# Kernel optimization log

Measured on AMD Instinct MI355X. Metric: run time of the kernel, lower is better.

## Reference

```python
import jax, jax.numpy as jnp
import numpy as np

NUM_NEIGHBORS = 10
BN_EPS = 1e-5


def setup_inputs() -> dict:
    key = jax.random.key(0)
    ks = jax.random.split(key, 6)
    B, N, D = 8, 4096, 64
    x = jax.random.normal(ks[0], (B, N, D), jnp.float32)

    def w(k, shape):
        return jax.random.normal(k, shape, jnp.float32) * 0.05

    return {
        "x": x,
        "gamma": jnp.ones((D,), jnp.float32),
        "beta": jnp.zeros((D,), jnp.float32),
        "W1": w(ks[1], (128, 128)), "b1": jnp.zeros((128,), jnp.float32),
        "W2": w(ks[2], (128, 64)), "b2": jnp.zeros((64,), jnp.float32),
        "W3": w(ks[3], (64, 64)), "b3": jnp.zeros((64,), jnp.float32),
        "Wg": w(ks[4], (128, 64)), "bg": jnp.zeros((64,), jnp.float32),
    }


def reference(x, gamma, beta, W1, b1, W2, b2, W3, b3, Wg, bg):
    B, N, D = x.shape
    K = NUM_NEIGHBORS

    # BatchNorm1d in train mode: normalize over all B*N rows with batch stats
    xf = x.reshape(-1, D)
    mu = jnp.mean(xf, axis=0)
    var = jnp.mean((xf - mu) ** 2, axis=0)  # biased, as torch BN uses
    xn = (((xf - mu) / jnp.sqrt(var + BN_EPS)) * gamma + beta).reshape(B, N, D)

    # KNN in feature space (standard DGCNN gather_neighbours)
    sq = jnp.sum(xn * xn, axis=-1)  # [B,N]
    dist = sq[:, :, None] + sq[:, None, :] - 2.0 * jnp.einsum("bnd,bmd->bnm", xn, xn)
    _, idx = jax.lax.top_k(-dist, K)  # [B,N,K] indices of nearest (incl. self)

    # gather neighbor features: neigh[b,n,k,:] = xn[b, idx[b,n,k], :]
    neigh = jax.vmap(lambda f, i: f[i])(xn, idx)  # [B,N,K,D]

    exp = jnp.broadcast_to(xn[:, :, None, :], (B, N, K, D))
    edge = jnp.concatenate([exp, exp - neigh], axis=-1)  # [B,N,K,2D]

    h = jax.nn.relu(edge @ W1 + b1)
    h = jax.nn.relu(h @ W2 + b2)
    h = jax.nn.relu(h @ W3 + b3)  # [B,N,K,64]

    vert = jnp.max(h, axis=2)  # max over neighbors -> [B,N,64]
    g = jnp.max(vert, axis=1, keepdims=True)  # global max-pool [B,1,64]
    cat = jnp.concatenate([vert, jnp.broadcast_to(g, vert.shape)], axis=-1)  # [B,N,128]
    return jax.nn.relu(cat @ Wg + bg)  # [B,N,64]
```

## Files before the change

### kernel.cpp

```cpp
#include <hip/hip_runtime.h>
#include <hip/hip_fp16.h>
#include <float.h>

#define BB 8
#define NN 4096
#define DD 64
#define KNBR 10
#define ROWS (BB*NN)

typedef _Float16 f16x8 __attribute__((ext_vector_type(8)));
typedef float f32x4 __attribute__((ext_vector_type(4)));

__global__ void k_bn_stats(const float* __restrict__ x, float* __restrict__ stats) {
  __shared__ float ls[2][4][64];
  int d = threadIdx.x & 63;
  int g = threadIdx.x >> 6;
  float s = 0.f, s2 = 0.f;
  for (int r = blockIdx.x * 4 + g; r < ROWS; r += gridDim.x * 4) {
    float val = x[r * 64 + d];
    s += val;
    s2 = fmaf(val, val, s2);
  }
  ls[0][g][d] = s;
  ls[1][g][d] = s2;
  __syncthreads();
  if (g == 0) {
    atomicAdd(&stats[d],      ls[0][0][d] + ls[0][1][d] + ls[0][2][d] + ls[0][3][d]);
    atomicAdd(&stats[64 + d], ls[1][0][d] + ls[1][1][d] + ls[1][2][d] + ls[1][3][d]);
  }
}

__global__ void k_bn_finalize(const float* __restrict__ stats,
                              const float* __restrict__ gamma,
                              const float* __restrict__ beta,
                              float* __restrict__ ss) {
  int d = threadIdx.x;
  const float inv = 1.f / 32768.f;
  float mu  = stats[d] * inv;
  float var = stats[64 + d] * inv - mu * mu;
  float sc  = gamma[d] / sqrtf(var + 1e-5f);
  ss[d]      = sc;
  ss[64 + d] = beta[d] - mu * sc;
}

__global__ void k_normalize(const float* __restrict__ x, const float* __restrict__ ss,
                            float* __restrict__ xn, float* __restrict__ sq,
                            _Float16* __restrict__ xh, _Float16* __restrict__ xl) {
  int row = blockIdx.x * 4 + (threadIdx.x >> 6);
  int d = threadIdx.x & 63;
  int idx = row * 64 + d;
  float val = fmaf(x[idx], ss[d], ss[64 + d]);
  xn[idx] = val;
  _Float16 h = (_Float16)val;
  _Float16 l = (_Float16)(val - (float)h);
  xh[idx] = h;
  xl[idx] = l;
  float p = val * val;
  #pragma unroll
  for (int off = 32; off > 0; off >>= 1) p += __shfl_xor(p, off);
  if (d == 0) sq[row] = p;
}

__global__ __launch_bounds__(256, 2) void k_knn(const _Float16* __restrict__ xh,
                                                const _Float16* __restrict__ xl,
                                                const float* __restrict__ sq,
                                                int* __restrict__ knn) {
  __shared__ __align__(16) float lds[16640];
  const int tid = threadIdx.x;
  const int w = tid >> 6, lane = tid & 63;
  const int l15 = lane & 15, lg = lane >> 4;
  const int b = blockIdx.x >> 6;
  const int rowbase = (blockIdx.x & 63) << 6;
  const int bN = b * NN;
  const _Float16* __restrict__ xhb = xh + (size_t)bN * 64;
  const _Float16* __restrict__ xlb = xl + (size_t)bN * 64;

  char* wbase = (char*)lds + w * 16640;
  char* Bhi = wbase;
  char* Blo = wbase + 4096;
  float* Dw = (float*)(wbase + 8192);

  f16x8 Ah[4][2], Al[4][2];
  #pragma unroll
  for (int mt = 0; mt < 4; ++mt) {
    #pragma unroll
    for (int ks = 0; ks < 2; ++ks) {
      int r = rowbase + mt * 16 + l15;
      Ah[mt][ks] = *(const f16x8*)(xhb + r * 64 + ks * 32 + lg * 8);
      Al[mt][ks] = *(const f16x8*)(xlb + r * 64 + ks * 32 + lg * 8);
    }
  }

  float bd[10]; int bi[10];
  #pragma unroll
  for (int i = 0; i < 10; ++i) { bd[i] = FLT_MAX; bi[i] = 0; }

  int srow[4], scc[4];
  #pragma unroll
  for (int i = 0; i < 4; ++i) { int c = i * 64 + lane; srow[i] = c >> 3; scc[i] = c & 7; }

  f16x8 sh[4], sl[4];
  {
    int mb0 = w * 32;
    #pragma unroll
    for (int i = 0; i < 4; ++i) {
      sh[i] = *(const f16x8*)(xhb + (mb0 + srow[i]) * 64 + scc[i] * 8);
      sl[i] = *(const f16x8*)(xlb + (mb0 + srow[i]) * 64 + scc[i] * 8);
    }
  }

  float* Drow = Dw + lane * 33;

  #pragma unroll 1
  for (int t = 0; t < 32; ++t) {
    const int mb = (t * 4 + w) * 32;
    const int mb2 = (t < 31) ? ((t + 1) * 4 + w) * 32 : mb;
    float sqv0 = sq[bN + mb + l15];
    float sqv1 = sq[bN + mb + 16 + l15];
    #pragma unroll
    for (int i = 0; i < 4; ++i) {
      int off = srow[i] * 128 + 16 * (scc[i] ^ (srow[i] & 7));
      *(f16x8*)(Bhi + off) = sh[i];
      *(f16x8*)(Blo + off) = sl[i];
    }
    #pragma unroll
    for (int i = 0; i < 4; ++i) {
      sh[i] = *(const f16x8*)(xhb + (mb2 + srow[i]) * 64 + scc[i] * 8);
      sl[i] = *(const f16x8*)(xlb + (mb2 + srow[i]) * 64 + scc[i] * 8);
    }
    f16x8 Bh[2][2], Bl[2][2];
    #pragma unroll
    for (int nt = 0; nt < 2; ++nt) {
      #pragma unroll
      for (int ks = 0; ks < 2; ++ks) {
        int rr2 = nt * 16 + l15;
        int off = rr2 * 128 + 16 * ((ks * 4 + lg) ^ (rr2 & 7));
        Bh[nt][ks] = *(const f16x8*)(Bhi + off);
        Bl[nt][ks] = *(const f16x8*)(Blo + off);
      }
    }
    #pragma unroll
    for (int mt = 0; mt < 4; ++mt) {
      f32x4 a0 = {0.f, 0.f, 0.f, 0.f}, a1 = {0.f, 0.f, 0.f, 0.f};
      #pragma unroll
      for (int ks = 0; ks < 2; ++ks) {
        a0 = __builtin_amdgcn_mfma_f32_16x16x32_f16(Ah[mt][ks], Bh[0][ks], a0, 0, 0, 0);
        a1 = __builtin_amdgcn_mfma_f32_16x16x32_f16(Ah[mt][ks], Bh[1][ks], a1, 0, 0, 0);
        a0 = __builtin_amdgcn_mfma_f32_16x16x32_f16(Ah[mt][ks], Bl[0][ks], a0, 0, 0, 0);
        a1 = __builtin_amdgcn_mfma_f32_16x16x32_f16(Ah[mt][ks], Bl[1][ks], a1, 0, 0, 0);
        a0 = __builtin_amdgcn_mfma_f32_16x16x32_f16(Al[mt][ks], Bh[0][ks], a0, 0, 0, 0);
        a1 = __builtin_amdgcn_mfma_f32_16x16x32_f16(Al[mt][ks], Bh[1][ks], a1, 0, 0, 0);
      }
      int rw = mt * 16 + lg * 4;
      #pragma unroll
      for (int r2 = 0; r2 < 4; ++r2) {
        Dw[(rw + r2) * 33 + l15]      = fmaf(-2.f, a0[r2], sqv0);
        Dw[(rw + r2) * 33 + 16 + l15] = fmaf(-2.f, a1[r2], sqv1);
      }
    }
    #pragma unroll 4
    for (int mm = 0; mm < 32; ++mm) {
      float dv = Drow[mm];
      if (dv < bd[9]) {
        float cd = dv; int ci = bN + mb + mm;
        #pragma unroll
        for (int j = 0; j < 10; ++j) {
          bool swp = cd < bd[j];
          float tf = bd[j]; int ti = bi[j];
          bd[j] = swp ? cd : tf; bi[j] = swp ? ci : ti;
          cd = swp ? tf : cd;    ci = swp ? ti : ci;
        }
      }
    }
  }

  __syncthreads();
  float* md = lds;
  int*   mi = (int*)(lds + 2560);
  #pragma unroll
  for (int i = 0; i < 10; ++i) {
    md[(w * 64 + lane) * 10 + i] = bd[i];
    mi[(w * 64 + lane) * 10 + i] = bi[i];
  }
  __syncthreads();
  if (tid < 64) {
    float fd[10]; int fi[10];
    #pragma unroll
    for (int i = 0; i < 10; ++i) { fd[i] = FLT_MAX; fi[i] = 0; }
    for (int w2 = 0; w2 < 4; ++w2) {
      for (int kk = 0; kk < 10; ++kk) {
        float dd2 = md[(w2 * 64 + tid) * 10 + kk];
        int   ii2 = mi[(w2 * 64 + tid) * 10 + kk];
        if (dd2 < fd[9]) {
          float cd = dd2; int ci = ii2;
          #pragma unroll
          for (int j = 0; j < 10; ++j) {
            bool swp = cd < fd[j];
            float tf = fd[j]; int ti = fi[j];
            fd[j] = swp ? cd : tf; fi[j] = swp ? ci : ti;
            cd = swp ? tf : cd;    ci = swp ? ti : ci;
          }
        }
      }
    }
    #pragma unroll
    for (int kk = 0; kk < 10; ++kk)
      knn[(bN + rowbase + tid) * KNBR + kk] = fi[kk];
  }
}

__global__ void k_uv(const float* __restrict__ xn, const float* __restrict__ W1,
                     const float* __restrict__ b1, float* __restrict__ u,
                     float* __restrict__ v) {
  __shared__ float xs[64 * 64];
  const int tid = threadIdx.x;
  const int o = tid & 127;
  const bool isU = tid < 128;
  const int rowbase = blockIdx.x * 64;

  float wreg[64];
  #pragma unroll
  for (int d = 0; d < 64; ++d) {
    float bw = W1[(64 + d) * 128 + o];
    wreg[d] = isU ? (W1[d * 128 + o] + bw) : bw;
  }
  const float bb = isU ? b1[o] : 0.f;
  float* __restrict__ dst = isU ? u : v;

  {
    const float4* s4 = (const float4*)(xn + rowbase * 64);
    float4* d4 = (float4*)xs;
    #pragma unroll
    for (int i = 0; i < 4; ++i) d4[tid + 256 * i] = s4[tid + 256 * i];
  }
  __syncthreads();

  for (int r = 0; r < 64; ++r) {
    const float4* xr = (const float4*)(xs + r * 64);
    float a0 = bb, a1 = 0.f, a2 = 0.f, a3 = 0.f;
    #pragma unroll
    for (int q = 0; q < 16; ++q) {
      float4 xv = xr[q];
      a0 = fmaf(xv.x, wreg[4 * q + 0], a0);
      a1 = fmaf(xv.y, wreg[4 * q + 1], a1);
      a2 = fmaf(xv.z, wreg[4 * q + 2], a2);
      a3 = fmaf(xv.w, wreg[4 * q + 3], a3);
    }
    dst[(rowbase + r) * 128 + o] = (a0 + a1) + (a2 + a3);
  }
}

__global__ __launch_bounds__(256, 2) void k_edge(const float* __restrict__ uu,
                                                 const float* __restrict__ vv,
                                                 const int* __restrict__ knn,
                                                 const float* __restrict__ W2,
                                                 const float* __restrict__ b2,
                                                 const float* __restrict__ W3,
                                                 const float* __restrict__ b3,
                                                 float* __restrict__ vert) {
  __shared__ __align__(16) _Float16 W3Ts[64 * 72];
  __shared__ __align__(16) _Float16 h2buf[4][16 * 88];
  __shared__ int vmaxs[4][512];
  const int tid = threadIdx.x;
  const int w = tid >> 6, lane = tid & 63;
  const int l15 = lane & 15, lg = lane >> 4;

  for (int i = tid; i < 64 * 64; i += 256) {
    int o3 = i >> 6, k2 = i & 63;
    W3Ts[o3 * 72 + k2] = (_Float16)W3[k2 * 64 + o3];
  }
  f16x8 w2f[4][4];
  #pragma unroll
  for (int ks = 0; ks < 4; ++ks) {
    #pragma unroll
    for (int nt = 0; nt < 4; ++nt) {
      f16x8 t;
      #pragma unroll
      for (int j = 0; j < 8; ++j)
        t[j] = (_Float16)W2[(ks * 32 + lg * 8 + j) * 64 + nt * 16 + l15];
      w2f[ks][nt] = t;
    }
  }
  float bias2[4], bias3[4];
  #pragma unroll
  for (int nt = 0; nt < 4; ++nt) { bias2[nt] = b2[nt * 16 + l15]; bias3[nt] = b3[nt * 16 + l15]; }

  _Float16* h2w = h2buf[w];
  int* vmaxw = vmaxs[w];
  #pragma unroll
  for (int q = 0; q < 8; ++q) vmaxw[lane * 8 + q] = 0;
  __syncthreads();

  const int wgid = blockIdx.x * 4 + w;
  for (int j = 0; j < 4; ++j) {
    const int g = wgid * 4 + j;
    const int n0 = g * 8;
    const int ebase = n0 * KNBR;
    #pragma unroll 1
    for (int mt = 0; mt < 5; ++mt) {
      const int e = mt * 16 + l15;
      const int m = knn[ebase + e];
      const int n = n0 + e / 10;
      const float* Up = uu + (size_t)n * 128 + lg * 8;
      const float* Vp = vv + (size_t)m * 128 + lg * 8;
      f16x8 A[4];
      #pragma unroll
      for (int ks = 0; ks < 4; ++ks) {
        float4 ua = *(const float4*)(Up + ks * 32);
        float4 ub = *(const float4*)(Up + ks * 32 + 4);
        float4 va = *(const float4*)(Vp + ks * 32);
        float4 vb = *(const float4*)(Vp + ks * 32 + 4);
        f16x8 t;
        t[0] = (_Float16)fmaxf(ua.x - va.x, 0.f);
        t[1] = (_Float16)fmaxf(ua.y - va.y, 0.f);
        t[2] = (_Float16)fmaxf(ua.z - va.z, 0.f);
        t[3] = (_Float16)fmaxf(ua.w - va.w, 0.f);
        t[4] = (_Float16)fmaxf(ub.x - vb.x, 0.f);
        t[5] = (_Float16)fmaxf(ub.y - vb.y, 0.f);
        t[6] = (_Float16)fmaxf(ub.z - vb.z, 0.f);
        t[7] = (_Float16)fmaxf(ub.w - vb.w, 0.f);
        A[ks] = t;
      }
      f32x4 acc[4];
      #pragma unroll
      for (int nt = 0; nt < 4; ++nt) { float bbv = bias2[nt]; acc[nt] = (f32x4){bbv, bbv, bbv, bbv}; }
      #pragma unroll
      for (int ks = 0; ks < 4; ++ks) {
        #pragma unroll
        for (int nt = 0; nt < 4; ++nt)
          acc[nt] = __builtin_amdgcn_mfma_f32_16x16x32_f16(A[ks], w2f[ks][nt], acc[nt], 0, 0, 0);
      }
      #pragma unroll
      for (int nt = 0; nt < 4; ++nt) {
        #pragma unroll
        for (int r = 0; r < 4; ++r)
          h2w[(lg * 4 + r) * 88 + nt * 16 + l15] = (_Float16)fmaxf(acc[nt][r], 0.f);
      }
      f16x8 A3[2];
      #pragma unroll
      for (int ks2 = 0; ks2 < 2; ++ks2)
        A3[ks2] = *(const f16x8*)(h2w + l15 * 88 + ks2 * 32 + lg * 8);
      f32x4 c3[4];
      #pragma unroll
      for (int nt = 0; nt < 4; ++nt) { float bbv = bias3[nt]; c3[nt] = (f32x4){bbv, bbv, bbv, bbv}; }
      #pragma unroll
      for (int ks2 = 0; ks2 < 2; ++ks2) {
        #pragma unroll
        for (int nt = 0; nt < 4; ++nt) {
          f16x8 bf = *(const f16x8*)(W3Ts + (nt * 16 + l15) * 72 + ks2 * 32 + lg * 8);
          c3[nt] = __builtin_amdgcn_mfma_f32_16x16x32_f16(A3[ks2], bf, c3[nt], 0, 0, 0);
        }
      }
      #pragma unroll
      for (int nt = 0; nt < 4; ++nt) {
        #pragma unroll
        for (int r = 0; r < 4; ++r) {
          float val = fmaxf(c3[nt][r], 0.f);
          int e2 = mt * 16 + lg * 4 + r;
          int p = e2 / 10;
          atomicMax(&vmaxw[p * 64 + nt * 16 + l15], __float_as_int(val));
        }
      }
    }
    {
      int p2 = lane >> 3, c0 = (lane & 7) * 8;
      const int* vp = &vmaxw[p2 * 64 + c0];
      float4 r0, r1;
      r0.x = __int_as_float(vp[0]); r0.y = __int_as_float(vp[1]);
      r0.z = __int_as_float(vp[2]); r0.w = __int_as_float(vp[3]);
      r1.x = __int_as_float(vp[4]); r1.y = __int_as_float(vp[5]);
      r1.z = __int_as_float(vp[6]); r1.w = __int_as_float(vp[7]);
      *(float4*)(vert + (size_t)(n0 + p2) * 64 + c0) = r0;
      *(float4*)(vert + (size_t)(n0 + p2) * 64 + c0 + 4) = r1;
      #pragma unroll
      for (int q = 0; q < 8; ++q) vmaxw[lane * 8 + q] = 0;
    }
  }
}

__global__ void k_gmax(const float* __restrict__ vert, float* __restrict__ g) {
  __shared__ float red[4][64];
  int b = blockIdx.x >> 4, chunk = blockIdx.x & 15;
  int sub = threadIdx.x >> 6, o = threadIdx.x & 63;
  float vm = 0.f;
  for (int j = 0; j < 64; ++j) {
    int r = chunk * 256 + j * 4 + sub;
    vm = fmaxf(vm, vert[(b * NN + r) * 64 + o]);
  }
  red[sub][o] = vm;
  __syncthreads();
  if (sub == 0) {
    float mm = fmaxf(fmaxf(red[0][o], red[1][o]), fmaxf(red[2][o], red[3][o]));
    atomicMax((int*)&g[b * 64 + o], __float_as_int(mm));
  }
}

__global__ void k_gb(const float* __restrict__ g, const float* __restrict__ Wg,
                     const float* __restrict__ bg, float* __restrict__ gb) {
  int t = threadIdx.x;
  int b = t >> 6, o = t & 63;
  float acc = bg[o];
  #pragma unroll
  for (int i = 0; i < 64; ++i)
    acc = fmaf(g[b * 64 + i], Wg[(64 + i) * 64 + o], acc);
  gb[b * 64 + o] = acc;
}

__global__ void k_final(const float* __restrict__ vert, const float* __restrict__ Wg,
                        const float* __restrict__ gb, float* __restrict__ out) {
  __shared__ float Wgs[64 * 64];
  int tid = threadIdx.x, w = tid >> 6, lane = tid & 63;
  for (int i = tid; i < 4096; i += 256) Wgs[i] = Wg[i];
  __syncthreads();
  int gw = blockIdx.x * 4 + w;
  for (int j = 0; j < 4; ++j) {
    int n = gw + 8192 * j;
    int b = n >> 12;
    float vrow = vert[n * 64 + lane];
    float ac0 = gb[b * 64 + lane], ac1 = 0.f, ac2 = 0.f, ac3 = 0.f;
    #pragma unroll
    for (int i = 0; i < 64; i += 4) {
      ac0 = fmaf(__shfl(vrow, i),     Wgs[i * 64 + lane],       ac0);
      ac1 = fmaf(__shfl(vrow, i + 1), Wgs[(i + 1) * 64 + lane], ac1);
      ac2 = fmaf(__shfl(vrow, i + 2), Wgs[(i + 2) * 64 + lane], ac2);
      ac3 = fmaf(__shfl(vrow, i + 3), Wgs[(i + 3) * 64 + lane], ac3);
    }
    out[n * 64 + lane] = fmaxf((ac0 + ac1) + (ac2 + ac3), 0.f);
  }
}

extern "C" void kernel_launch(void* const* d_in, const int* in_sizes, int n_in,
                              void* d_out, int out_size, void* d_ws, size_t ws_size,
                              hipStream_t stream) {
  const float* x     = (const float*)d_in[0];
  const float* gamma = (const float*)d_in[1];
  const float* beta  = (const float*)d_in[2];
  const float* W1    = (const float*)d_in[3];
  const float* b1    = (const float*)d_in[4];
  const float* W2    = (const float*)d_in[5];
  const float* b2    = (const float*)d_in[6];
  const float* W3    = (const float*)d_in[7];
  const float* b3    = (const float*)d_in[8];
  const float* Wg    = (const float*)d_in[9];
  const float* bg    = (const float*)d_in[10];
  float* out = (float*)d_out;

  float* ws    = (float*)d_ws;
  float* stats = ws;
  float* ss    = ws + 128;
  float* xn    = ws + 256;
  float* sq    = xn + 2097152;
  int*   knn   = (int*)(sq + 32768);
  float* u     = (float*)(knn + 327680);
  float* v     = u + 4194304;
  float* vert  = v + 4194304;
  float* g     = vert + 2097152;
  float* gb    = g + 512;
  _Float16* xh = (_Float16*)(gb + 512);
  _Float16* xl = (_Float16*)(gb + 512 + 1048576);

  hipMemsetAsync(stats, 0, 128 * sizeof(float), stream);
  hipMemsetAsync(g, 0, 512 * sizeof(float), stream);

  k_bn_stats<<<256, 256, 0, stream>>>(x, stats);
  k_bn_finalize<<<1, 64, 0, stream>>>(stats, gamma, beta, ss);
  k_normalize<<<8192, 256, 0, stream>>>(x, ss, xn, sq, xh, xl);
  k_knn<<<512, 256, 0, stream>>>(xh, xl, sq, knn);
  k_uv<<<512, 256, 0, stream>>>(xn, W1, b1, u, v);
  k_edge<<<256, 256, 0, stream>>>(u, v, knn, W2, b2, W3, b3, vert);
  k_gmax<<<128, 256, 0, stream>>>(vert, g);
  k_gb<<<1, 512, 0, stream>>>(g, Wg, bg, gb);
  k_final<<<2048, 256, 0, stream>>>(vert, Wg, gb, out);
}
```

Measured before the change: 474.9 us.

## Track only top-k distances, then recompute pass to emit neighbor indices

The per-lane top-10 insertion now keeps only distance values, using a branchless min/max network instead of paired value/index swaps, and the cross-wave merge drops index arrays. The 10th-smallest distance becomes a per-row threshold. A second full pass recomputes the MFMA distance tiles and writes every candidate at or below the threshold into the knn output through shared-memory atomic slot counters. This cuts register pressure and the cost of the selection loop, but doubles the distance GEMM work. Neighbor order becomes nondeterministic, and ties at the threshold may drop indices.

Result: no change. 469.3 us (-1.2%).

```diff
diff --git a/kernel.cpp b/kernel.cpp
--- a/kernel.cpp
+++ b/kernel.cpp
@@ -66,6 +66,8 @@
                                                 const float* __restrict__ sq,
                                                 int* __restrict__ knn) {
   __shared__ __align__(16) float lds[16640];
+  __shared__ float thrs[64];
+  __shared__ int cnts[64];
   const int tid = threadIdx.x;
   const int w = tid >> 6, lane = tid & 63;
   const int l15 = lane & 15, lg = lane >> 4;
@@ -91,9 +93,9 @@
     }
   }
 
-  float bd[10]; int bi[10];
-  #pragma unroll
-  for (int i = 0; i < 10; ++i) { bd[i] = FLT_MAX; bi[i] = 0; }
+  float bd[10];
+  #pragma unroll
+  for (int i = 0; i < 10; ++i) bd[i] = FLT_MAX;
 
   int srow[4], scc[4];
   #pragma unroll
@@ -160,15 +162,15 @@
     }
     #pragma unroll 4
     for (int mm = 0; mm < 32; ++mm) {
-      float dv = Drow[mm];
-      if (dv < bd[9]) {
-        float cd = dv; int ci = bN + mb + mm;
+      float cd = Drow[mm];
+      if (cd < bd[9]) {
+        float prev = bd[0];
+        bd[0] = fminf(cd, bd[0]);
         #pragma unroll
-        for (int j = 0; j < 10; ++j) {
-          bool swp = cd < bd[j];
-          float tf = bd[j]; int ti = bi[j];
-          bd[j] = swp ? cd : tf; bi[j] = swp ? ci : ti;
-          cd = swp ? tf : cd;    ci = swp ? ti : ci;
+        for (int j = 1; j < 10; ++j) {
+          float cur = bd[j];
+          bd[j] = fminf(cur, fmaxf(prev, cd));
+          prev = cur;
         }
       }
     }
@@ -176,36 +178,106 @@
 
   __syncthreads();
   float* md = lds;
-  int*   mi = (int*)(lds + 2560);
-  #pragma unroll
-  for (int i = 0; i < 10; ++i) {
-    md[(w * 64 + lane) * 10 + i] = bd[i];
-    mi[(w * 64 + lane) * 10 + i] = bi[i];
-  }
+  #pragma unroll
+  for (int i = 0; i < 10; ++i) md[(w * 64 + lane) * 10 + i] = bd[i];
+  if (tid < 64) cnts[tid] = 0;
   __syncthreads();
   if (tid < 64) {
-    float fd[10]; int fi[10];
-    #pragma unroll
-    for (int i = 0; i < 10; ++i) { fd[i] = FLT_MAX; fi[i] = 0; }
+    float fd[10];
+    #pragma unroll
+    for (int i = 0; i < 10; ++i) fd[i] = FLT_MAX;
     for (int w2 = 0; w2 < 4; ++w2) {
+      #pragma unroll
       for (int kk = 0; kk < 10; ++kk) {
-        float dd2 = md[(w2 * 64 + tid) * 10 + kk];
-        int   ii2 = mi[(w2 * 64 + tid) * 10 + kk];
-        if (dd2 < fd[9]) {
-          float cd = dd2; int ci = ii2;
+        float cd = md[(w2 * 64 + tid) * 10 + kk];
+        if (cd < fd[9]) {
+          float prev = fd[0];
+          fd[0] = fminf(cd, fd[0]);
           #pragma unroll
-          for (int j = 0; j < 10; ++j) {
-            bool swp = cd < fd[j];
-            float tf = fd[j]; int ti = fi[j];
-            fd[j] = swp ? cd : tf; fi[j] = swp ? ci : ti;
-            cd = swp ? tf : cd;    ci = swp ? ti : ci;
+          for (int j = 1; j < 10; ++j) {
+            float cur = fd[j];
+            fd[j] = fminf(cur, fmaxf(prev, cd));
+            prev = cur;
           }
         }
       }
     }
-    #pragma unroll
-    for (int kk = 0; kk < 10; ++kk)
-      knn[(bN + rowbase + tid) * KNBR + kk] = fi[kk];
+    thrs[tid] = fd[9];
+  }
+  __syncthreads();
+
+  float thv[4][4];
+  #pragma unroll
+  for (int mt = 0; mt < 4; ++mt)
+    #pragma unroll
+    for (int r2 = 0; r2 < 4; ++r2)
+      thv[mt][r2] = thrs[mt * 16 + lg * 4 + r2];
+
+  int* knnrow = knn + (size_t)(bN + rowbase) * KNBR;
+
+  {
+    int mb0 = w * 32;
+    #pragma unroll
+    for (int i = 0; i < 4; ++i) {
+      sh[i] = *(const f16x8*)(xhb + (mb0 + srow[i]) * 64 + scc[i] * 8);
+      sl[i] = *(const f16x8*)(xlb + (mb0 + srow[i]) * 64 + scc[i] * 8);
+    }
+  }
+  #pragma unroll 1
+  for (int t = 0; t < 32; ++t) {
+    const int mb = (t * 4 + w) * 32;
+    const int mb2 = (t < 31) ? ((t + 1) * 4 + w) * 32 : mb;
+    float sqv0 = sq[bN + mb + l15];
+    float sqv1 = sq[bN + mb + 16 + l15];
+    #pragma unroll
+    for (int i = 0; i < 4; ++i) {
+      int off = srow[i] * 128 + 16 * (scc[i] ^ (srow[i] & 7));
+      *(f16x8*)(Bhi + off) = sh[i];
+      *(f16x8*)(Blo + off) = sl[i];
+    }
+    #pragma unroll
+    for (int i = 0; i < 4; ++i) {
+      sh[i] = *(const f16x8*)(xhb + (mb2 + srow[i]) * 64 + scc[i] * 8);
+      sl[i] = *(const f16x8*)(xlb + (mb2 + srow[i]) * 64 + scc[i] * 8);
+    }
+    f16x8 Bh[2][2], Bl[2][2];
+    #pragma unroll
+    for (int nt = 0; nt < 2; ++nt) {
+      #pragma unroll
+      for (int ks = 0; ks < 2; ++ks) {
+        int rr2 = nt * 16 + l15;
+        int off = rr2 * 128 + 16 * ((ks * 4 + lg) ^ (rr2 & 7));
+        Bh[nt][ks] = *(const f16x8*)(Bhi + off);
+        Bl[nt][ks] = *(const f16x8*)(Blo + off);
+      }
+    }
+    #pragma unroll
+    for (int mt = 0; mt < 4; ++mt) {
+      f32x4 a0 = {0.f, 0.f, 0.f, 0.f}, a1 = {0.f, 0.f, 0.f, 0.f};
+      #pragma unroll
+      for (int ks = 0; ks < 2; ++ks) {
+        a0 = __builtin_amdgcn_mfma_f32_16x16x32_f16(Ah[mt][ks], Bh[0][ks], a0, 0, 0, 0);
+        a1 = __builtin_amdgcn_mfma_f32_16x16x32_f16(Ah[mt][ks], Bh[1][ks], a1, 0, 0, 0);
+        a0 = __builtin_amdgcn_mfma_f32_16x16x32_f16(Ah[mt][ks], Bl[0][ks], a0, 0, 0, 0);
+        a1 = __builtin_amdgcn_mfma_f32_16x16x32_f16(Ah[mt][ks], Bl[1][ks], a1, 0, 0, 0);
+        a0 = __builtin_amdgcn_mfma_f32_16x16x32_f16(Al[mt][ks], Bh[0][ks], a0, 0, 0, 0);
+        a1 = __builtin_amdgcn_mfma_f32_16x16x32_f16(Al[mt][ks], Bh[1][ks], a1, 0, 0, 0);
+      }
+      #pragma unroll
+      for (int r2 = 0; r2 < 4; ++r2) {
+        float d0 = fmaf(-2.f, a0[r2], sqv0);
+        float d1 = fmaf(-2.f, a1[r2], sqv1);
+        int row = mt * 16 + lg * 4 + r2;
+        if (d0 <= thv[mt][r2]) {
+          int slot = atomicAdd(&cnts[row], 1);
+          if (slot < KNBR) knnrow[row * KNBR + slot] = bN + mb + l15;
+        }
+        if (d1 <= thv[mt][r2]) {
+          int slot = atomicAdd(&cnts[row], 1);
+          if (slot < KNBR) knnrow[row * KNBR + slot] = bN + mb + 16 + l15;
+        }
+      }
+    }
   }
 }
 
```

## Restructure KNN into two-pass threshold search with register-resident distance tiles

Applied to the files above, without the earlier changes.

The KNN kernel now computes distances with candidate rows as the MFMA A operand, so each lane holds 4 distances for one query column directly in registers, with no LDS staging of B tiles or the distance matrix. A first pass keeps only distance values in a fminf/fmaxf insertion network to find each query's 10th-smallest distance threshold. A second pass recomputes the distances and writes the indices at or below the threshold through LDS atomic counters. This drops per-element index bookkeeping and LDS traffic and raises occupancy to 3 blocks per CU, at the cost of doubling the MFMA work. It also drops the ordering of neighbours and the tie handling, which is safe only because the later max over neighbours does not depend on order.

After: 499.2 us. 1.05x slower.

```diff
diff --git a/kernel.cpp b/kernel.cpp
--- a/kernel.cpp
+++ b/kernel.cpp
@@ -61,11 +61,13 @@
   if (d == 0) sq[row] = p;
 }
 
-__global__ __launch_bounds__(256, 2) void k_knn(const _Float16* __restrict__ xh,
+__global__ __launch_bounds__(256, 3) void k_knn(const _Float16* __restrict__ xh,
                                                 const _Float16* __restrict__ xl,
                                                 const float* __restrict__ sq,
                                                 int* __restrict__ knn) {
-  __shared__ __align__(16) float lds[16640];
+  __shared__ float md[64 * 16 * 10];
+  __shared__ float thrs[64];
+  __shared__ int cnts[64];
   const int tid = threadIdx.x;
   const int w = tid >> 6, lane = tid & 63;
   const int l15 = lane & 15, lg = lane >> 4;
@@ -74,138 +76,147 @@
   const int bN = b * NN;
   const _Float16* __restrict__ xhb = xh + (size_t)bN * 64;
   const _Float16* __restrict__ xlb = xl + (size_t)bN * 64;
-
-  char* wbase = (char*)lds + w * 16640;
-  char* Bhi = wbase;
-  char* Blo = wbase + 4096;
-  float* Dw = (float*)(wbase + 8192);
-
-  f16x8 Ah[4][2], Al[4][2];
-  #pragma unroll
-  for (int mt = 0; mt < 4; ++mt) {
+  const float* __restrict__ sqb = sq + bN;
+
+  f16x8 Qh[4][2], Ql[4][2];
+  #pragma unroll
+  for (int nt = 0; nt < 4; ++nt) {
     #pragma unroll
     for (int ks = 0; ks < 2; ++ks) {
-      int r = rowbase + mt * 16 + l15;
-      Ah[mt][ks] = *(const f16x8*)(xhb + r * 64 + ks * 32 + lg * 8);
-      Al[mt][ks] = *(const f16x8*)(xlb + r * 64 + ks * 32 + lg * 8);
-    }
-  }
-
-  float bd[10]; int bi[10];
-  #pragma unroll
-  for (int i = 0; i < 10; ++i) { bd[i] = FLT_MAX; bi[i] = 0; }
-
-  int srow[4], scc[4];
-  #pragma unroll
-  for (int i = 0; i < 4; ++i) { int c = i * 64 + lane; srow[i] = c >> 3; scc[i] = c & 7; }
-
-  f16x8 sh[4], sl[4];
-  {
-    int mb0 = w * 32;
-    #pragma unroll
-    for (int i = 0; i < 4; ++i) {
-      sh[i] = *(const f16x8*)(xhb + (mb0 + srow[i]) * 64 + scc[i] * 8);
-      sl[i] = *(const f16x8*)(xlb + (mb0 + srow[i]) * 64 + scc[i] * 8);
-    }
-  }
-
-  float* Drow = Dw + lane * 33;
+      int qrow = rowbase + nt * 16 + l15;
+      Qh[nt][ks] = *(const f16x8*)(xhb + qrow * 64 + ks * 32 + lg * 8);
+      Ql[nt][ks] = *(const f16x8*)(xlb + qrow * 64 + ks * 32 + lg * 8);
+    }
+  }
+
+  float bd[4][10];
+  #pragma unroll
+  for (int nt = 0; nt < 4; ++nt)
+    #pragma unroll
+    for (int i = 0; i < 10; ++i) bd[nt][i] = FLT_MAX;
+
+  const int mbase0 = w * 1024;
 
   #pragma unroll 1
   for (int t = 0; t < 32; ++t) {
-    const int mb = (t * 4 + w) * 32;
-    const int mb2 = (t < 31) ? ((t + 1) * 4 + w) * 32 : mb;
-    float sqv0 = sq[bN + mb + l15];
-    float sqv1 = sq[bN + mb + 16 + l15];
-    #pragma unroll
-    for (int i = 0; i < 4; ++i) {
-      int off = srow[i] * 128 + 16 * (scc[i] ^ (srow[i] & 7));
-      *(f16x8*)(Bhi + off) = sh[i];
-      *(f16x8*)(Blo + off) = sl[i];
-    }
-    #pragma unroll
-    for (int i = 0; i < 4; ++i) {
-      sh[i] = *(const f16x8*)(xhb + (mb2 + srow[i]) * 64 + scc[i] * 8);
-      sl[i] = *(const f16x8*)(xlb + (mb2 + srow[i]) * 64 + scc[i] * 8);
-    }
-    f16x8 Bh[2][2], Bl[2][2];
-    #pragma unroll
-    for (int nt = 0; nt < 2; ++nt) {
+    const int mb = mbase0 + t * 32;
+    f16x8 Mh[2][2], Ml[2][2];
+    #pragma unroll
+    for (int mt = 0; mt < 2; ++mt) {
       #pragma unroll
       for (int ks = 0; ks < 2; ++ks) {
-        int rr2 = nt * 16 + l15;
-        int off = rr2 * 128 + 16 * ((ks * 4 + lg) ^ (rr2 & 7));
-        Bh[nt][ks] = *(const f16x8*)(Bhi + off);
-        Bl[nt][ks] = *(const f16x8*)(Blo + off);
-      }
-    }
-    #pragma unroll
-    for (int mt = 0; mt < 4; ++mt) {
-      f32x4 a0 = {0.f, 0.f, 0.f, 0.f}, a1 = {0.f, 0.f, 0.f, 0.f};
+        int mrow = mb + mt * 16 + l15;
+        Mh[mt][ks] = *(const f16x8*)(xhb + mrow * 64 + ks * 32 + lg * 8);
+        Ml[mt][ks] = *(const f16x8*)(xlb + mrow * 64 + ks * 32 + lg * 8);
+      }
+    }
+    f32x4 sqv[2];
+    sqv[0] = *(const f32x4*)(sqb + mb + lg * 4);
+    sqv[1] = *(const f32x4*)(sqb + mb + 16 + lg * 4);
+    #pragma unroll
+    for (int nt = 0; nt < 4; ++nt) {
+      #pragma unroll
+      for (int mt = 0; mt < 2; ++mt) {
+        f32x4 a = {0.f, 0.f, 0.f, 0.f};
+        #pragma unroll
+        for (int ks = 0; ks < 2; ++ks) {
+          a = __builtin_amdgcn_mfma_f32_16x16x32_f16(Mh[mt][ks], Qh[nt][ks], a, 0, 0, 0);
+          a = __builtin_amdgcn_mfma_f32_16x16x32_f16(Mh[mt][ks], Ql[nt][ks], a, 0, 0, 0);
+          a = __builtin_amdgcn_mfma_f32_16x16x32_f16(Ml[mt][ks], Qh[nt][ks], a, 0, 0, 0);
+        }
+        #pragma unroll
+        for (int r = 0; r < 4; ++r) {
+          float cd = fmaf(-2.f, a[r], sqv[mt][r]);
+          if (cd < bd[nt][9]) {
+            float prev = bd[nt][0];
+            bd[nt][0] = fminf(cd, bd[nt][0]);
+            #pragma unroll
+            for (int j = 1; j < 10; ++j) {
+              float cur = bd[nt][j];
+              bd[nt][j] = fminf(cur, fmaxf(prev, cd));
+              prev = cur;
+            }
+          }
+        }
+      }
+    }
+  }
+
+  #pragma unroll
+  for (int nt = 0; nt < 4; ++nt)
+    #pragma unroll
+    for (int i = 0; i < 10; ++i)
+      md[((nt * 16 + l15) * 16 + (w * 4 + lg)) * 10 + i] = bd[nt][i];
+  if (tid < 64) cnts[tid] = 0;
+  __syncthreads();
+  if (tid < 64) {
+    float fd[10];
+    #pragma unroll
+    for (int i = 0; i < 10; ++i) fd[i] = FLT_MAX;
+    for (int li = 0; li < 16; ++li) {
+      #pragma unroll 1
+      for (int kk = 0; kk < 10; ++kk) {
+        float cd = md[(tid * 16 + li) * 10 + kk];
+        if (cd < fd[9]) {
+          float prev = fd[0];
+          fd[0] = fminf(cd, fd[0]);
+          #pragma unroll
+          for (int j = 1; j < 10; ++j) {
+            float cur = fd[j];
+            fd[j] = fminf(cur, fmaxf(prev, cd));
+            prev = cur;
+          }
+        } else break;
+      }
+    }
+    thrs[tid] = fd[9];
+  }
+  __syncthreads();
+
+  float thv[4];
+  #pragma unroll
+  for (int nt = 0; nt < 4; ++nt) thv[nt] = thrs[nt * 16 + l15];
+  int* knnrow = knn + (size_t)(bN + rowbase) * KNBR;
+
+  #pragma unroll 1
+  for (int t = 0; t < 32; ++t) {
+    const int mb = mbase0 + t * 32;
+    f16x8 Mh[2][2], Ml[2][2];
+    #pragma unroll
+    for (int mt = 0; mt < 2; ++mt) {
       #pragma unroll
       for (int ks = 0; ks < 2; ++ks) {
-        a0 = __builtin_amdgcn_mfma_f32_16x16x32_f16(Ah[mt][ks], Bh[0][ks], a0, 0, 0, 0);
-        a1 = __builtin_amdgcn_mfma_f32_16x16x32_f16(Ah[mt][ks], Bh[1][ks], a1, 0, 0, 0);
-        a0 = __builtin_amdgcn_mfma_f32_16x16x32_f16(Ah[mt][ks], Bl[0][ks], a0, 0, 0, 0);
-        a1 = __builtin_amdgcn_mfma_f32_16x16x32_f16(Ah[mt][ks], Bl[1][ks], a1, 0, 0, 0);
-        a0 = __builtin_amdgcn_mfma_f32_16x16x32_f16(Al[mt][ks], Bh[0][ks], a0, 0, 0, 0);
-        a1 = __builtin_amdgcn_mfma_f32_16x16x32_f16(Al[mt][ks], Bh[1][ks], a1, 0, 0, 0);
-      }
-      int rw = mt * 16 + lg * 4;
-      #pragma unroll
-      for (int r2 = 0; r2 < 4; ++r2) {
-        Dw[(rw + r2) * 33 + l15]      = fmaf(-2.f, a0[r2], sqv0);
-        Dw[(rw + r2) * 33 + 16 + l15] = fmaf(-2.f, a1[r2], sqv1);
-      }
-    }
-    #pragma unroll 4
-    for (int mm = 0; mm < 32; ++mm) {
-      float dv = Drow[mm];
-      if (dv < bd[9]) {
-        float cd = dv; int ci = bN + mb + mm;
-        #pragma unroll
-        for (int j = 0; j < 10; ++j) {
-          bool swp = cd < bd[j];
-          float tf = bd[j]; int ti = bi[j];
-          bd[j] = swp ? cd : tf; bi[j] = swp ? ci : ti;
-          cd = swp ? tf : cd;    ci = swp ? ti : ci;
-        }
-      }
-    }
-  }
-
-  __syncthreads();
-  float* md = lds;
-  int*   mi = (int*)(lds + 2560);
-  #pragma unroll
-  for (int i = 0; i < 10; ++i) {
-    md[(w * 64 + lane) * 10 + i] = bd[i];
-    mi[(w * 64 + lane) * 10 + i] = bi[i];
-  }
-  __syncthreads();
-  if (tid < 64) {
-    float fd[10]; int fi[10];
-    #pragma unroll
-    for (int i = 0; i < 10; ++i) { fd[i] = FLT_MAX; fi[i] = 0; }
-    for (int w2 = 0; w2 < 4; ++w2) {
-      for (int kk = 0; kk < 10; ++kk) {
-        float dd2 = md[(w2 * 64 + tid) * 10 + kk];
-        int   ii2 = mi[(w2 * 64 + tid) * 10 + kk];
-        if (dd2 < fd[9]) {
-          float cd = dd2; int ci = ii2;
-          #pragma unroll
-          for (int j = 0; j < 10; ++j) {
-            bool swp = cd < fd[j];
-            float tf = fd[j]; int ti = fi[j];
-            fd[j] = swp ? cd : tf; fi[j] = swp ? ci : ti;
-            cd = swp ? tf : cd;    ci = swp ? ti : ci;
+        int mrow = mb + mt * 16 + l15;
+        Mh[mt][ks] = *(const f16x8*)(xhb + mrow * 64 + ks * 32 + lg * 8);
+        Ml[mt][ks] = *(const f16x8*)(xlb + mrow * 64 + ks * 32 + lg * 8);
+      }
+    }
+    f32x4 sqv[2];
+    sqv[0] = *(const f32x4*)(sqb + mb + lg * 4);
+    sqv[1] = *(const f32x4*)(sqb + mb + 16 + lg * 4);
+    #pragma unroll
+    for (int nt = 0; nt < 4; ++nt) {
+      #pragma unroll
+      for (int mt = 0; mt < 2; ++mt) {
+        f32x4 a = {0.f, 0.f, 0.f, 0.f};
+        #pragma unroll
+        for (int ks = 0; ks < 2; ++ks) {
+          a = __builtin_amdgcn_mfma_f32_16x16x32_f16(Mh[mt][ks], Qh[nt][ks], a, 0, 0, 0);
+          a = __builtin_amdgcn_mfma_f32_16x16x32_f16(Mh[mt][ks], Ql[nt][ks], a, 0, 0, 0);
+          a = __builtin_amdgcn_mfma_f32_16x16x32_f16(Ml[mt][ks], Qh[nt][ks], a, 0, 0, 0);
+        }
+        #pragma unroll
+        for (int r = 0; r < 4; ++r) {
+          float cd = fmaf(-2.f, a[r], sqv[mt][r]);
+          if (cd <= thv[nt]) {
+            int qi = nt * 16 + l15;
+            int slot = atomicAdd(&cnts[qi], 1);
+            if (slot < KNBR)
+              knnrow[qi * KNBR + slot] = bN + mb + mt * 16 + lg * 4 + r;
           }
         }
       }
     }
-    #pragma unroll
-    for (int kk = 0; kk < 10; ++kk)
-      knn[(bN + rowbase + tid) * KNBR + kk] = fi[kk];
   }
 }
 
```
